# Performance work log

Hardware: AMD Instinct MI355X
Metric: run time of the kernel (lower is better)

Reference implementation:

```python
import jax, jax.numpy as jnp
import numpy as np

C = 256
SHAPE = (4, 256, 32, 32, 32)  # B, C, D, H, W


def setup_inputs() -> dict:
    key = jax.random.key(0)
    ks = jax.random.split(key, 8)
    scale = 1.0 / np.sqrt(C)
    return {
        "x": jax.random.normal(ks[0], SHAPE, dtype=jnp.float32),
        "y": jax.random.normal(ks[1], SHAPE, dtype=jnp.float32),
        "Wq": jax.random.normal(ks[2], (C, C), dtype=jnp.float32) * scale,
        "bq": jax.random.normal(ks[3], (C,), dtype=jnp.float32) * 0.01,
        "Wk": jax.random.normal(ks[4], (C, C), dtype=jnp.float32) * scale,
        "bk": jax.random.normal(ks[5], (C,), dtype=jnp.float32) * 0.01,
        "Wv": jax.random.normal(ks[6], (C, C), dtype=jnp.float32) * scale,
        "bv": jax.random.normal(ks[7], (C,), dtype=jnp.float32) * 0.01,
    }


def _proj_flat(v, W, b):
    # 1x1x1 Conv3d == per-voxel linear over channels. v: [B,C,D,H,W] -> [B,C,N]
    B, Cc = v.shape[0], v.shape[1]
    vf = v.reshape(B, Cc, -1)  # [B, C, N]
    return jnp.einsum("oc,bcn->bon", W, vf) + b[None, :, None]


def reference(x, y, Wq, bq, Wk, bk, Wv, bv):
    spatial = y.shape[2:]
    q = _proj_flat(x, Wq, bq)  # [B, C, N]
    k = _proj_flat(y, Wk, bk)  # [B, C, N]
    v = _proj_flat(y, Wv, bv)  # [B, C, N]
    # channel-attention: scores[b, i, j] = sum_n q[b,i,n] * k[b,j,n]  (unscaled)
    scores = jnp.einsum("bin,bjn->bij", q, k)  # [B, C, C]
    weights = jax.nn.softmax(scores, axis=2)
    fused = jnp.einsum("bij,bjn->bin", weights, v)  # [B, C, N]
    return fused.reshape(fused.shape[0], fused.shape[1], *spatial)
```

## Files before the change

kernel.cpp:

```cpp
#include <hip/hip_runtime.h>

#define Bb 4
#define Cc 256
#define Nn 32768

typedef short s16x8 __attribute__((ext_vector_type(8)));
typedef float f32x4 __attribute__((ext_vector_type(4)));
typedef float f32x4v __attribute__((ext_vector_type(4)));

__device__ __forceinline__ unsigned short bfh(float f) {
    union { float f; unsigned u; } c; c.f = f;
    unsigned u = c.u + 0x7fffu + ((c.u >> 16) & 1u);
    return (unsigned short)(u >> 16);
}
__device__ __forceinline__ unsigned fbits(float f) {
    union { float f; unsigned u; } c; c.f = f; return c.u;
}
__device__ __forceinline__ float fof(unsigned u) {
    union { unsigned u; float f; } c; c.u = u; return c.f;
}
__device__ __forceinline__ int swz(int l) { return l ^ ((l >> 3) & 6); }

__device__ __forceinline__ void cvt8(f32x4v A, f32x4v B, uint4& h, uint4& l) {
    unsigned a0 = fbits(A.x), a1 = fbits(A.y), a2 = fbits(A.z), a3 = fbits(A.w);
    unsigned b0 = fbits(B.x), b1 = fbits(B.y), b2 = fbits(B.z), b3 = fbits(B.w);
    h.x = __builtin_amdgcn_perm(a1, a0, 0x07060302u);
    h.y = __builtin_amdgcn_perm(a3, a2, 0x07060302u);
    h.z = __builtin_amdgcn_perm(b1, b0, 0x07060302u);
    h.w = __builtin_amdgcn_perm(b3, b2, 0x07060302u);
    unsigned l0 = fbits(A.x - fof(a0 & 0xffff0000u)) + 0x8000u;
    unsigned l1 = fbits(A.y - fof(a1 & 0xffff0000u)) + 0x8000u;
    unsigned l2 = fbits(A.z - fof(a2 & 0xffff0000u)) + 0x8000u;
    unsigned l3 = fbits(A.w - fof(a3 & 0xffff0000u)) + 0x8000u;
    unsigned m0 = fbits(B.x - fof(b0 & 0xffff0000u)) + 0x8000u;
    unsigned m1 = fbits(B.y - fof(b1 & 0xffff0000u)) + 0x8000u;
    unsigned m2 = fbits(B.z - fof(b2 & 0xffff0000u)) + 0x8000u;
    unsigned m3 = fbits(B.w - fof(b3 & 0xffff0000u)) + 0x8000u;
    l.x = __builtin_amdgcn_perm(l1, l0, 0x07060302u);
    l.y = __builtin_amdgcn_perm(l3, l2, 0x07060302u);
    l.z = __builtin_amdgcn_perm(m1, m0, 0x07060302u);
    l.w = __builtin_amdgcn_perm(m3, m2, 0x07060302u);
}
__device__ __forceinline__ float s4(f32x4v v) { return (v.x + v.y) + (v.z + v.w); }

__global__ __launch_bounds__(512, 2) void k_gram(const float* __restrict__ x,
                                                 const float* __restrict__ y,
                                                 float* __restrict__ part,
                                                 float* __restrict__ sxp,
                                                 float* __restrict__ syp,
                                                 int nsplit) {
    extern __shared__ short smem[];

    int G = Bb * nsplit * 2;
    int chunk = G >> 3;
    int lid = blockIdx.x;
    int bid = (lid & 7) * chunk + (lid >> 3);

    int half = bid & 1;
    int ks = (bid >> 1) % nsplit;
    int b = bid / (2 * nsplit);
    int Kblk = Nn / nsplit;
    int nstep = Kblk >> 5;

    const float* X = x + (size_t)b * Cc * Nn + (size_t)(half * 128) * Nn + (size_t)ks * Kblk;
    const float* Y = y + (size_t)b * Cc * Nn + (size_t)ks * Kblk;

    int tid = threadIdx.x;
    int lane = tid & 63;
    int wave = tid >> 6;
    int wr = wave >> 2, wc = wave & 3;

    int xr = tid >> 2, xq = tid & 3;
    const float* px = X + (size_t)xr * Nn + xq * 8;
    int xl = (xr & 15) + 16 * xq;
    int xo = ((xr >> 4) * 64 + swz(xl)) * 8;
    int yr = tid >> 1, yh2 = tid & 1;
    const float* py = Y + (size_t)yr * Nn + yh2 * 16;
    int yl0 = (yr & 15) + 32 * yh2, yl1 = yl0 + 16;
    int yo0 = ((yr >> 4) * 64 + swz(yl0)) * 8;
    int yo1 = ((yr >> 4) * 64 + swz(yl1)) * 8;

    f32x4 acc[4][4];
    #pragma unroll
    for (int i = 0; i < 4; ++i)
        #pragma unroll
        for (int j = 0; j < 4; ++j)
            #pragma unroll
            for (int z = 0; z < 4; ++z) acc[i][j][z] = 0.f;

    float xsum = 0.f, ysum = 0.f;
    f32x4v A0[2], B0[4], A1[2], B1[4];

    #define LDX(A, B, kb) do { \
        A[0] = __builtin_nontemporal_load((const f32x4v*)(px + (kb)) + 0); \
        A[1] = __builtin_nontemporal_load((const f32x4v*)(px + (kb)) + 1); \
        B[0] = ((const f32x4v*)(py + (kb)))[0]; B[1] = ((const f32x4v*)(py + (kb)))[1]; \
        B[2] = ((const f32x4v*)(py + (kb)))[2]; B[3] = ((const f32x4v*)(py + (kb)))[3]; \
    } while (0)

    #define COMPUTE(Sb) do { \
        int sl = swz(lane); \
        s16x8 ah[4], al[4]; \
        _Pragma("unroll") \
        for (int i = 0; i < 4; ++i) { \
            int fr = (wr * 4 + i) * 64 + sl; \
            ah[i] = *(const s16x8*)&(Sb)[fr * 8]; \
            al[i] = *(const s16x8*)&(Sb)[4096 + fr * 8]; \
        } \
        _Pragma("unroll") \
        for (int j = 0; j < 4; ++j) { \
            int fr = (wc * 4 + j) * 64 + sl; \
            s16x8 bh = *(const s16x8*)&(Sb)[8192 + fr * 8]; \
            s16x8 bl = *(const s16x8*)&(Sb)[16384 + fr * 8]; \
            _Pragma("unroll") \
            for (int i = 0; i < 4; ++i) { \
                acc[i][j] = __builtin_amdgcn_mfma_f32_16x16x32_bf16(ah[i], bh, acc[i][j], 0, 0, 0); \
                acc[i][j] = __builtin_amdgcn_mfma_f32_16x16x32_bf16(ah[i], bl, acc[i][j], 0, 0, 0); \
                acc[i][j] = __builtin_amdgcn_mfma_f32_16x16x32_bf16(al[i], bh, acc[i][j], 0, 0, 0); \
            } \
        } \
    } while (0)

    #define GSTEP(A, B, nkb, donext, cur) do { \
        uint4 hx, qxv, hy0, qy0, hy1, qy1; \
        cvt8(A[0], A[1], hx, qxv); \
        cvt8(B[0], B[1], hy0, qy0); \
        cvt8(B[2], B[3], hy1, qy1); \
        xsum += s4(A[0]) + s4(A[1]); \
        if (half == 0) ysum += s4(B[0]) + s4(B[1]) + s4(B[2]) + s4(B[3]); \
        short* Sb = smem + (cur); \
        *(uint4*)&Sb[xo] = hx;  *(uint4*)&Sb[4096 + xo] = qxv; \
        *(uint4*)&Sb[8192 + yo0] = hy0; *(uint4*)&Sb[16384 + yo0] = qy0; \
        *(uint4*)&Sb[8192 + yo1] = hy1; *(uint4*)&Sb[16384 + yo1] = qy1; \
        if (donext) LDX(A, B, nkb); \
        asm volatile("s_waitcnt lgkmcnt(0)" ::: "memory"); \
        __builtin_amdgcn_sched_barrier(0); \
        __builtin_amdgcn_s_barrier(); \
        __builtin_amdgcn_sched_barrier(0); \
        COMPUTE(Sb); \
    } while (0)

    LDX(A0, B0, 0);
    LDX(A1, B1, 32);
    for (int t = 0; t < nstep; t += 2) {
        GSTEP(A0, B0, (t + 2) * 32, t + 2 < nstep, 0);
        GSTEP(A1, B1, (t + 3) * 32, t + 3 < nstep, 24576);
    }
    #undef GSTEP
    #undef COMPUTE
    #undef LDX

    xsum += __shfl_xor(xsum, 1);
    xsum += __shfl_xor(xsum, 2);
    ysum += __shfl_xor(ysum, 1);
    if (xq == 0) sxp[((size_t)b * nsplit + ks) * 256 + half * 128 + xr] = xsum;
    if (half == 0 && yh2 == 0) syp[((size_t)b * nsplit + ks) * 256 + yr] = ysum;

    float* P = part + ((size_t)b * nsplit + ks) * Cc * Cc;
    #pragma unroll
    for (int i = 0; i < 4; ++i)
        #pragma unroll
        for (int j = 0; j < 4; ++j)
            #pragma unroll
            for (int reg = 0; reg < 4; ++reg) {
                int gi = half * 128 + wr * 64 + i * 16 + (lane >> 4) * 4 + reg;
                int gj = wc * 64 + j * 16 + (lane & 15);
                P[(size_t)gi * Cc + gj] = acc[i][j][reg];
            }
}

__global__ __launch_bounds__(256) void k_reduceS(const float* __restrict__ part,
                                                 const float* __restrict__ sxp,
                                                 const float* __restrict__ syp,
                                                 float* __restrict__ S,
                                                 float* __restrict__ sx,
                                                 float* __restrict__ sy, int split) {
    if (blockIdx.x < 256) {
        int t = blockIdx.x * 256 + threadIdx.x;
        int b = t >> 14;
        int rc = t & 16383;
        f32x4v s = {0.f, 0.f, 0.f, 0.f};
        for (int ks = 0; ks < split; ++ks) {
            f32x4v v = __builtin_nontemporal_load(
                (const f32x4v*)(part + (((size_t)b * split + ks) << 16)) + rc);
            s += v;
        }
        ((f32x4v*)S)[t] = s;
    } else {
        int flat = (blockIdx.x - 256) * 256 + threadIdx.x;
        int b = flat >> 9, rem = flat & 511, which = rem >> 8, c = rem & 255;
        const float* src = (which ? syp : sxp) + (size_t)b * split * 256 + c;
        float s = 0.f;
        for (int ks = 0; ks < split; ++ks)
            s += __builtin_nontemporal_load(src + (size_t)ks * 256);
        (which ? sy : sx)[b * 256 + c] = s;
    }
}

__global__ __launch_bounds__(256) void k_attn(const float* __restrict__ S,
                                              const float* __restrict__ sx,
                                              const float* __restrict__ sy,
                                              const float* __restrict__ Wq,
                                              const float* __restrict__ Wk,
                                              const float* __restrict__ Wv,
                                              const float* __restrict__ bq,
                                              const float* __restrict__ bk,
                                              const float* __restrict__ bv,
                                              short* __restrict__ Mbf,
                                              float* __restrict__ cb) {
    __shared__ float wq_lds[8][256];
    __shared__ float u_lds[8][256];
    __shared__ float p_lds[8][256];
    __shared__ float wv_lds[32][256];
    __shared__ float sx_lds[256], sy_lds[256];
    __shared__ float qx_lds[8];

    int b = blockIdx.x >> 5;
    int i0 = (blockIdx.x & 31) << 3;
    int tid = threadIdx.x;
    int lane = tid & 63, wv4 = tid >> 6;

    float bqv[8];
    #pragma unroll
    for (int ii = 0; ii < 8; ++ii) {
        wq_lds[ii][tid] = Wq[(size_t)(i0 + ii) * Cc + tid];
        bqv[ii] = bq[i0 + ii];
    }
    sx_lds[tid] = sx[b * Cc + tid];
    sy_lds[tid] = sy[b * Cc + tid];
    __syncthreads();

    float u[8] = {};
    const float* Sb = S + (size_t)b * Cc * Cc + tid;
    #pragma unroll 4
    for (int c = 0; c < Cc; ++c) {
        float s = Sb[(size_t)c * Cc];
        #pragma unroll
        for (int ii = 0; ii < 8; ++ii) u[ii] += wq_lds[ii][c] * s;
    }
    #pragma unroll
    for (int ii = 0; ii < 8; ++ii) u_lds[ii][tid] = u[ii] + bqv[ii] * sy_lds[tid];

    #pragma unroll
    for (int rr = 0; rr < 2; ++rr) {
        int ii = wv4 * 2 + rr;
        float p = 0.f;
        #pragma unroll
        for (int k = 0; k < 4; ++k) { int c = lane + 64 * k; p += wq_lds[ii][c] * sx_lds[c]; }
        #pragma unroll
        for (int m = 1; m < 64; m <<= 1) p += __shfl_xor(p, m);
        if (lane == 0) qx_lds[ii] = p;
    }
    __syncthreads();

    float sc[8] = {};
    const float* WkRow = Wk + (size_t)tid * Cc;
    for (int ch = 0; ch < 8; ++ch) {
        float wkr[32];
        #pragma unroll
        for (int k = 0; k < 8; ++k)
            *(float4*)&wkr[4 * k] = ((const float4*)(WkRow + ch * 32))[k];
        #pragma unroll
        for (int dd = 0; dd < 32; ++dd) {
            float w = wkr[dd];
            #pragma unroll
            for (int ii = 0; ii < 8; ++ii) sc[ii] += u_lds[ii][ch * 32 + dd] * w;
        }
    }
    float bkj = bk[tid];
    #pragma unroll
    for (int ii = 0; ii < 8; ++ii) {
        sc[ii] += (qx_lds[ii] + 32768.0f * bqv[ii]) * bkj;
        p_lds[ii][tid] = sc[ii];
    }
    __syncthreads();

    #pragma unroll
    for (int rr = 0; rr < 2; ++rr) {
        int ii = wv4 * 2 + rr;
        float v0 = p_lds[ii][lane], v1 = p_lds[ii][lane + 64];
        float v2 = p_lds[ii][lane + 128], v3 = p_lds[ii][lane + 192];
        float mx = fmaxf(fmaxf(v0, v1), fmaxf(v2, v3));
        #pragma unroll
        for (int m = 1; m < 64; m <<= 1) mx = fmaxf(mx, __shfl_xor(mx, m));
        float e0 = expf(v0 - mx), e1 = expf(v1 - mx), e2 = expf(v2 - mx), e3 = expf(v3 - mx);
        float ssum = (e0 + e1) + (e2 + e3);
        #pragma unroll
        for (int m = 1; m < 64; m <<= 1) ssum += __shfl_xor(ssum, m);
        float inv = 1.0f / ssum;
        float w0 = e0 * inv, w1 = e1 * inv, w2 = e2 * inv, w3 = e3 * inv;
        p_lds[ii][lane] = w0; p_lds[ii][lane + 64] = w1;
        p_lds[ii][lane + 128] = w2; p_lds[ii][lane + 192] = w3;
        float cbp = w0 * bv[lane] + w1 * bv[lane + 64] + w2 * bv[lane + 128] + w3 * bv[lane + 192];
        #pragma unroll
        for (int m = 1; m < 64; m <<= 1) cbp += __shfl_xor(cbp, m);
        if (lane == 0) cb[b * Cc + i0 + ii] = cbp;
    }
    __syncthreads();

    float m[8] = {};
    for (int jc = 0; jc < 8; ++jc) {
        #pragma unroll
        for (int k = 0; k < 8; ++k) {
            int fidx = k * 256 + tid;
            int jj = fidx >> 6, f4 = fidx & 63;
            *(float4*)&wv_lds[jj][4 * f4] =
                *(const float4*)(Wv + (size_t)(jc * 32 + jj) * Cc + 4 * f4);
        }
        __syncthreads();
        #pragma unroll 4
        for (int jj = 0; jj < 32; ++jj) {
            float w = wv_lds[jj][tid];
            #pragma unroll
            for (int ii = 0; ii < 8; ++ii) m[ii] += p_lds[ii][jc * 32 + jj] * w;
        }
        __syncthreads();
    }
    #pragma unroll
    for (int ii = 0; ii < 8; ++ii)
        Mbf[((size_t)(b * Cc + i0 + ii)) * Cc + tid] = (short)bfh(m[ii]);
}

__global__ __launch_bounds__(512, 2) void k_out_mfma(const short* __restrict__ Mbf,
                                                     const float* __restrict__ y,
                                                     const float* __restrict__ cb,
                                                     float* __restrict__ out) {
    int tid = threadIdx.x;
    int lane = tid & 63;
    int wave = tid >> 6;
    int wr = wave >> 2, wc = wave & 3;
    int bid = blockIdx.x;
    int b = bid >> 8, grp = bid & 255;
    int nbase = grp * 128 + wc * 32;
    const float* Y = y + (size_t)b * Cc * Nn;
    const short* M = Mbf + (size_t)b * Cc * Cc;
    int l15 = lane & 15;
    int cbase = 8 * (lane >> 4);
    int n0 = nbase + l15;

    f32x4 acc[8][2];
    #pragma unroll
    for (int ti = 0; ti < 8; ++ti)
        #pragma unroll
        for (int nb = 0; nb < 2; ++nb)
            #pragma unroll
            for (int z = 0; z < 4; ++z) acc[ti][nb][z] = 0.f;

    s16x8 af0[8], af1[8];
    float ya0[8], yb0[8], ya1[8], yb1[8];

    #define AFLD(AF, s) do { int c0 = 32 * (s) + cbase; \
        _Pragma("unroll") \
        for (int ti = 0; ti < 8; ++ti) \
            AF[ti] = *(const s16x8*)&M[(size_t)(wr * 128 + ti * 16 + l15) * Cc + c0]; \
        } while (0)

    #define LDY(YA, YB, s) do { int c0 = 32 * (s) + cbase; \
        _Pragma("unroll") \
        for (int j = 0; j < 8; ++j) { \
            YA[j] = Y[(size_t)(c0 + j) * Nn + n0]; \
            YB[j] = Y[(size_t)(c0 + j) * Nn + n0 + 16]; \
        } } while (0)

    #define OSTEP(AF, AFN, YA, YB, s) do { \
        s16x8 bf0, bf1; \
        _Pragma("unroll") \
        for (int j = 0; j < 8; ++j) { bf0[j] = (short)bfh(YA[j]); bf1[j] = (short)bfh(YB[j]); } \
        if ((s) + 1 < 8) AFLD(AFN, (s) + 1); \
        if ((s) + 2 < 8) LDY(YA, YB, (s) + 2); \
        _Pragma("unroll") \
        for (int ti = 0; ti < 8; ++ti) { \
            acc[ti][0] = __builtin_amdgcn_mfma_f32_16x16x32_bf16(AF[ti], bf0, acc[ti][0], 0, 0, 0); \
            acc[ti][1] = __builtin_amdgcn_mfma_f32_16x16x32_bf16(AF[ti], bf1, acc[ti][1], 0, 0, 0); \
        } } while (0)

    AFLD(af0, 0);
    LDY(ya0, yb0, 0);
    LDY(ya1, yb1, 1);
    for (int s = 0; s < 8; s += 2) {
        OSTEP(af0, af1, ya0, yb0, s);
        OSTEP(af1, af0, ya1, yb1, s + 1);
    }
    #undef OSTEP
    #undef LDY
    #undef AFLD

    #pragma unroll
    for (int ti = 0; ti < 8; ++ti)
        #pragma unroll
        for (int nb = 0; nb < 2; ++nb)
            #pragma unroll
            for (int reg = 0; reg < 4; ++reg) {
                int i = wr * 128 + ti * 16 + (lane >> 4) * 4 + reg;
                out[((size_t)b * Cc + i) * Nn + nbase + nb * 16 + l15] =
                    acc[ti][nb][reg] + cb[b * Cc + i];
            }
}

extern "C" void kernel_launch(void* const* d_in, const int* in_sizes, int n_in,
                              void* d_out, int out_size, void* d_ws, size_t ws_size,
                              hipStream_t stream) {
    const float* x  = (const float*)d_in[0];
    const float* y  = (const float*)d_in[1];
    const float* Wq = (const float*)d_in[2];
    const float* bq = (const float*)d_in[3];
    const float* Wk = (const float*)d_in[4];
    const float* bk = (const float*)d_in[5];
    const float* Wv = (const float*)d_in[6];
    const float* bv = (const float*)d_in[7];
    float* out = (float*)d_out;

    float* ws = (float*)d_ws;
    size_t off = 0;
    float* S  = ws + off; off += (size_t)Bb * Cc * Cc;
    float* sx = ws + off; off += Bb * Cc;
    float* sy = ws + off; off += Bb * Cc;
    short* Mbf = (short*)(ws + off); off += (size_t)Bb * Cc * Cc / 2;
    float* cb = ws + off; off += Bb * Cc;
    float* sxp = ws + off; off += (size_t)Bb * 64 * 256;
    float* syp = ws + off; off += (size_t)Bb * 64 * 256;
    float* part = ws + off;

    size_t avail = ws_size / 4 - off;
    int split = 32;
    while (split > 16 && (size_t)split * Bb * Cc * Cc > avail) split >>= 1;

    (void)hipFuncSetAttribute(reinterpret_cast<const void*>(k_gram),
                              hipFuncAttributeMaxDynamicSharedMemorySize, 98304);

    k_gram<<<Bb * split * 2, 512, 98304, stream>>>(x, y, part, sxp, syp, split);
    k_reduceS<<<264, 256, 0, stream>>>(part, sxp, syp, S, sx, sy, split);
    k_attn<<<Bb * 32, 256, 0, stream>>>(S, sx, sy, Wq, Wk, Wv, bq, bk, bv, Mbf, cb);
    k_out_mfma<<<1024, 512, 0, stream>>>(Mbf, y, cb, out);
}
```

Before: 220.2 us.

## Stage y tiles into LDS via async global_load_lds with double buffering

In the output GEMM kernel, each wave now copies its 32x32 y tile per k-step into a per-wave, double-buffered LDS region using direct global-to-LDS 16-byte loads. A XOR swizzle avoids bank conflicts. This replaces scalar strided 4-byte global loads held in registers with wide coalesced loads and fewer VGPRs. It relies on a hand-placed vmcnt wait and a sched_barrier, and the 64KB of LDS per block may limit occupancy.

```diff
diff --git a/kernel.cpp b/kernel.cpp
--- a/kernel.cpp
+++ b/kernel.cpp
@@ -20,6 +20,10 @@
     union { unsigned u; float f; } c; c.u = u; return c.f;
 }
 __device__ __forceinline__ int swz(int l) { return l ^ ((l >> 3) & 6); }
+
+#define GLOAD16(g, l) __builtin_amdgcn_global_load_lds( \
+    (const __attribute__((address_space(1))) void*)(g), \
+    (__attribute__((address_space(3))) void*)(l), 16, 0, 0)
 
 __device__ __forceinline__ void cvt8(f32x4v A, f32x4v B, uint4& h, uint4& l) {
     unsigned a0 = fbits(A.x), a1 = fbits(A.y), a2 = fbits(A.z), a3 = fbits(A.w);
@@ -325,6 +329,8 @@
                                                      const float* __restrict__ y,
                                                      const float* __restrict__ cb,
                                                      float* __restrict__ out) {
+    __shared__ float ylds[16384];
+
     int tid = threadIdx.x;
     int lane = tid & 63;
     int wave = tid >> 6;
@@ -334,9 +340,18 @@
     int nbase = grp * 128 + wc * 32;
     const float* Y = y + (size_t)b * Cc * Nn;
     const short* M = Mbf + (size_t)b * Cc * Cc;
-    int l15 = lane & 15;
-    int cbase = 8 * (lane >> 4);
-    int n0 = nbase + l15;
+    int l15 = lane & 15, lh = lane >> 4;
+    int cbase = 8 * lh;
+    int wbase = wave * 2048;
+
+    const float* ysrc[4];
+    #pragma unroll
+    for (int k = 0; k < 4; ++k) {
+        int u = k * 64 + lane;
+        int c = u >> 3;
+        int key = (c >> 3) << 1;
+        ysrc[k] = Y + (size_t)c * Nn + nbase + (((u & 7) ^ key) << 2);
+    }
 
     f32x4 acc[8][2];
     #pragma unroll
@@ -347,7 +362,13 @@
             for (int z = 0; z < 4; ++z) acc[ti][nb][z] = 0.f;
 
     s16x8 af0[8], af1[8];
-    float ya0[8], yb0[8], ya1[8], yb1[8];
+
+    #define STAGE(buf, s) do { \
+        _Pragma("unroll") \
+        for (int k = 0; k < 4; ++k) \
+            GLOAD16(ysrc[k] + (size_t)(32 * (s)) * Nn, \
+                    &ylds[wbase + (buf) * 1024 + k * 256]); \
+        } while (0)
 
     #define AFLD(AF, s) do { int c0 = 32 * (s) + cbase; \
         _Pragma("unroll") \
@@ -355,35 +376,39 @@
             AF[ti] = *(const s16x8*)&M[(size_t)(wr * 128 + ti * 16 + l15) * Cc + c0]; \
         } while (0)
 
-    #define LDY(YA, YB, s) do { int c0 = 32 * (s) + cbase; \
+    #define OSTEP(AF, buf) do { \
+        asm volatile("s_waitcnt vmcnt(8)" ::: "memory"); \
+        __builtin_amdgcn_sched_barrier(0); \
+        int rb = wbase + (buf) * 1024; \
+        int rkey = lh << 1; \
+        s16x8 bf0, bf1; \
         _Pragma("unroll") \
         for (int j = 0; j < 8; ++j) { \
-            YA[j] = Y[(size_t)(c0 + j) * Nn + n0]; \
-            YB[j] = Y[(size_t)(c0 + j) * Nn + n0 + 16]; \
-        } } while (0)
-
-    #define OSTEP(AF, AFN, YA, YB, s) do { \
-        s16x8 bf0, bf1; \
-        _Pragma("unroll") \
-        for (int j = 0; j < 8; ++j) { bf0[j] = (short)bfh(YA[j]); bf1[j] = (short)bfh(YB[j]); } \
-        if ((s) + 1 < 8) AFLD(AFN, (s) + 1); \
-        if ((s) + 2 < 8) LDY(YA, YB, (s) + 2); \
+            float f0 = ylds[rb + (cbase + j) * 32 + (((l15 >> 2) ^ rkey) << 2) + (l15 & 3)]; \
+            float f1 = ylds[rb + (cbase + j) * 32 + ((((l15 >> 2) + 4) ^ rkey) << 2) + (l15 & 3)]; \
+            bf0[j] = (short)bfh(f0); \
+            bf1[j] = (short)bfh(f1); \
+        } \
         _Pragma("unroll") \
         for (int ti = 0; ti < 8; ++ti) { \
             acc[ti][0] = __builtin_amdgcn_mfma_f32_16x16x32_bf16(AF[ti], bf0, acc[ti][0], 0, 0, 0); \
             acc[ti][1] = __builtin_amdgcn_mfma_f32_16x16x32_bf16(AF[ti], bf1, acc[ti][1], 0, 0, 0); \
         } } while (0)
 
+    STAGE(0, 0);
+    STAGE(1, 1);
     AFLD(af0, 0);
-    LDY(ya0, yb0, 0);
-    LDY(ya1, yb1, 1);
     for (int s = 0; s < 8; s += 2) {
-        OSTEP(af0, af1, ya0, yb0, s);
-        OSTEP(af1, af0, ya1, yb1, s + 1);
+        OSTEP(af0, 0);
+        if (s + 1 < 8) AFLD(af1, s + 1);
+        if (s + 2 < 8) STAGE(0, s + 2);
+        OSTEP(af1, 1);
+        if (s + 2 < 8) AFLD(af0, s + 2);
+        if (s + 3 < 8) STAGE(1, s + 3);
     }
     #undef OSTEP
-    #undef LDY
     #undef AFLD
+    #undef STAGE
 
     #pragma unroll
     for (int ti = 0; ti < 8; ++ti)
```

New measurement: 218.4 us, median of 2. Within noise of the previous version (-0.8%).
